# Optimization experiments

Hardware: AMD Instinct MI355X
Metric: run time of the kernel (lower is better)

## Reference

```python
import jax, jax.numpy as jnp
import numpy as np

NUM_HEADS = 12

def _rotate_half(t):
    t1, t2 = jnp.split(t, 2, axis=-1)
    return jnp.concatenate([-t2, t1], axis=-1)

def _rope_apply(t, sin, cos):
    # t: [B,H,N,Dh]; sin/cos: [N,Dh] broadcast over B,H
    return t * cos + _rotate_half(t) * sin


def setup_inputs() -> dict:
    key = jax.random.key(0)
    ks = jax.random.split(key, 6)
    B, N, D = 2, 2048, 768
    Dh = D // NUM_HEADS
    return {
        "x": jax.random.normal(ks[0], (B, N, D), dtype=jnp.float32),
        "sin": jax.random.uniform(ks[1], (N, Dh), dtype=jnp.float32),
        "cos": jax.random.uniform(ks[2], (N, Dh), dtype=jnp.float32),
        "qkv_w": jax.random.normal(ks[3], (3 * D, D), dtype=jnp.float32) * (D ** -0.5),
        "proj_w": jax.random.normal(ks[4], (D, D), dtype=jnp.float32) * (D ** -0.5),
        "proj_b": jax.random.normal(ks[5], (D,), dtype=jnp.float32),
    }


def reference(x, sin, cos, qkv_w, proj_w, proj_b):
    B, N, D = x.shape
    H = NUM_HEADS
    Dh = D // H
    scale = Dh ** -0.5
    # fused QKV projection (qkv_bias=False)
    qkv = jnp.einsum("bnd,ed->bne", x, qkv_w)              # [B,N,3D]
    qkv = qkv.reshape(B, N, 3, H, Dh)
    q = jnp.transpose(qkv[:, :, 0], (0, 2, 1, 3))          # [B,H,N,Dh]
    k = jnp.transpose(qkv[:, :, 1], (0, 2, 1, 3))
    v = jnp.transpose(qkv[:, :, 2], (0, 2, 1, 3))
    # inline RoPE (prefix = 0: sin/cos cover all N positions)
    q = _rope_apply(q, sin, cos)
    k = _rope_apply(k, sin, cos)
    # scaled dot-product attention
    scores = jnp.einsum("bhqd,bhkd->bhqk", q, k) * scale   # [B,H,N,N]
    attn = jax.nn.softmax(scores, axis=-1)
    out = jnp.einsum("bhqk,bhkd->bhqd", attn, v)           # [B,H,N,Dh]
    out = jnp.transpose(out, (0, 2, 1, 3)).reshape(B, N, D)
    # output projection
    return jnp.einsum("bnd,ed->bne", out, proj_w) + proj_b
```

## Files before the change

### kernel.cpp

```cpp
#include <hip/hip_runtime.h>
#include <hip/hip_bf16.h>
#include <stdint.h>


typedef unsigned short u16;
typedef __attribute__((ext_vector_type(8))) short s16x8;
typedef __attribute__((ext_vector_type(4))) short s16x4;
typedef __attribute__((ext_vector_type(4))) float f32x4;

#define MFMA16(a, b, c) __builtin_amdgcn_mfma_f32_16x16x32_bf16((a), (b), (c), 0, 0, 0)

__device__ __forceinline__ f32x4 mfma_k16(s16x4 a, s16x4 b, f32x4 c) {
    asm("s_nop 3\n\tv_mfma_f32_16x16x16_bf16 %0, %1, %2, %0"
        : "+v"(c) : "v"(a), "v"(b));
    return c;
}

__device__ __forceinline__ u16 f2bf(float f) {
    uint32_t u = __float_as_uint(f);
    u = u + 0x7fffu + ((u >> 16) & 1u);
    return (u16)(u >> 16);
}
__device__ __forceinline__ uint32_t pk2(float lo, float hi) {
    return (uint32_t)f2bf(lo) | ((uint32_t)f2bf(hi) << 16);
}
__device__ __forceinline__ uint32_t pk2t(float lo, float hi) {
    return __builtin_amdgcn_perm(__float_as_uint(hi), __float_as_uint(lo),
                                 0x07060302u);
}
__device__ __forceinline__ float fexp2(float x) { return __builtin_amdgcn_exp2f(x); }

__device__ __forceinline__ void gload16(const void* g, void* l) {
    __builtin_amdgcn_global_load_lds(
        (const __attribute__((address_space(1))) unsigned int*)g,
        (__attribute__((address_space(3))) unsigned int*)l,
        16, 0, 0);
}

__global__ __launch_bounds__(256)
void k_cvt3(const float* __restrict__ s0, const float* __restrict__ s1,
            const float* __restrict__ s2, u16* __restrict__ dst,
            int a, int ab, int tot)
{
    const int i = blockIdx.x * 256 + threadIdx.x;
    if (i >= tot) return;
    const float4* src;
    if (i < a)       src = (const float4*)s0 + i;
    else if (i < ab) src = (const float4*)s1 + (i - a);
    else             src = (const float4*)s2 + (i - ab);
    const float4 v = *src;
    ushort4 o;
    o.x = f2bf(v.x); o.y = f2bf(v.y); o.z = f2bf(v.z); o.w = f2bf(v.w);
    ((ushort4*)dst)[i] = o;
}

__global__ __launch_bounds__(256, 2)
void k_qkv_rope(const u16* __restrict__ X,
                const u16* __restrict__ W,
                const float* __restrict__ SIN,
                const float* __restrict__ COS,
                u16* __restrict__ qws, u16* __restrict__ kws, u16* __restrict__ vtws)
{
    __shared__ u16 smem[17408];
    u16* const As0 = smem;
    u16* const Bs0 = smem + 8192;

    const int t  = threadIdx.x;
    const int l  = t & 63;
    const int w  = t >> 6;
    const int cl = l & 15, gh = l >> 4;
    const int brow = blockIdx.x * 128;
    const int bcol = blockIdx.y * 128;
    const int wr = (w >> 1) * 64;
    const int wc = (w & 1) * 64;

    const int srow = w * 16 + (l >> 2);
    const int scol = (((l & 3) ^ ((l >> 3) & 3)) * 8);
    const u16* gA = X + (size_t)(brow + srow) * 768 + scol;
    const u16* gB = W + (size_t)(bcol + srow) * 768 + scol;

    const int csw = ((cl >> 1) & 3);

    f32x4 acc[4][4] = {};

    gload16(gA,            As0 + w * 512);
    gload16(gA + 64 * 768, As0 + 2048 + w * 512);
    gload16(gB,            Bs0 + w * 512);
    gload16(gB + 64 * 768, Bs0 + 2048 + w * 512);
    __syncthreads();

    for (int kt = 0; kt < 24; ++kt) {
        const int cur = kt & 1;
        if (kt + 1 < 24) {
            const int k0 = (kt + 1) * 32;
            u16* An = As0 + (cur ^ 1) * 4096;
            u16* Bn = Bs0 + (cur ^ 1) * 4096;
            gload16(gA + k0,            An + w * 512);
            gload16(gA + k0 + 64 * 768, An + 2048 + w * 512);
            gload16(gB + k0,            Bn + w * 512);
            gload16(gB + k0 + 64 * 768, Bn + 2048 + w * 512);
        }
        const char* Ac = (const char*)(As0 + cur * 4096);
        const char* Bc = (const char*)(Bs0 + cur * 4096);
        s16x8 af[4], bv[4];
        #pragma unroll
        for (int m = 0; m < 4; ++m) {
            const int row = wr + m * 16 + cl;
            af[m] = *(const s16x8*)(Ac + row * 64 + ((gh ^ csw) << 4));
        }
        #pragma unroll
        for (int n = 0; n < 4; ++n) {
            const int row = wc + n * 16 + cl;
            bv[n] = *(const s16x8*)(Bc + row * 64 + ((gh ^ csw) << 4));
        }
        #pragma unroll
        for (int m = 0; m < 4; ++m)
            #pragma unroll
            for (int n = 0; n < 4; ++n)
                acc[m][n] = MFMA16(af[m], bv[n], acc[m][n]);
        __syncthreads();
    }

    if (blockIdx.y >= 12) {
        u16* const Vt = smem;
        #pragma unroll
        for (int m = 0; m < 4; ++m)
            #pragma unroll
            for (int jj = 0; jj < 4; ++jj) {
                const int rowl = wr + m * 16 + gh * 4 + jj;
                #pragma unroll
                for (int n = 0; n < 4; ++n)
                    Vt[(wc + n * 16 + cl) * 136 + rowl] = f2bf(acc[m][n][jj]);
            }
        __syncthreads();
        const int dhcol = t >> 1;
        const int c     = t & 1;
        const int gcol  = bcol + dhcol;
        const int h     = (gcol >> 6) - 24;
        const int dh    = gcol & 63;
        const int b     = brow >> 11;
        const int tok0  = (brow & 2047) + c * 64;
        u16* dst = vtws + ((size_t)(b * 12 + h) * 64 + dh) * 2048 + tok0;
        const uint4* src = (const uint4*)((const char*)Vt + dhcol * 272 + c * 128);
        #pragma unroll
        for (int j = 0; j < 8; ++j)
            ((uint4*)dst)[j] = src[j];
    } else {
        const int seg   = (bcol + wc) >> 6;
        const int which = seg / 12;
        const int h     = seg % 12;
        const float qscl = (which == 0) ? 0.1803368801111244f : 1.0f;
        u16* outp = (which == 0) ? qws : kws;

        #pragma unroll
        for (int m = 0; m < 4; ++m) {
            #pragma unroll
            for (int jj = 0; jj < 4; ++jj) {
                const int row = brow + wr + m * 16 + gh * 4 + jj;
                const int b   = row >> 11;
                const int tok = row & 2047;
                u16* orow = outp + ((size_t)(b * 12 + h) * 2048 + tok) * 64;
                const float* srow2 = SIN + tok * 64;
                const float* crow2 = COS + tok * 64;
                #pragma unroll
                for (int n = 0; n < 4; ++n) {
                    const int dh = n * 16 + cl;
                    const float v = acc[m][n][jj];
                    const float partner = (n < 2) ? -acc[m][n + 2][jj] : acc[m][n - 2][jj];
                    orow[dh] = f2bf((v * crow2[dh] + partner * srow2[dh]) * qscl);
                }
            }
        }
    }
}

__global__ __launch_bounds__(256, 3)
void k_attn(const u16* __restrict__ Qg, const u16* __restrict__ Kg,
            const u16* __restrict__ VTg, u16* __restrict__ Og)
{
    __shared__ u16 Ks[2][64 * 64];
    __shared__ u16 Vs[2][64 * 64];

    const int t  = threadIdx.x;
    const int l  = t & 63;
    const int w  = t >> 6;
    const int cl = l & 15, gh = l >> 4;

    const int i  = blockIdx.x;
    const int bh = (i & 7) * 3 + ((i >> 3) % 3);
    const int qt = i / 24;
    const int qb = qt * 64;

    const u16* Q  = Qg  + (size_t)bh * 2048 * 64;
    const char* Kb  = (const char*)(Kg  + (size_t)bh * 2048 * 64);
    const char* VTb = (const char*)(VTg + (size_t)bh * 64 * 2048);

    s16x8 qf[4][2];
    #pragma unroll
    for (int m = 0; m < 4; ++m)
        #pragma unroll
        for (int ks = 0; ks < 2; ++ks)
            qf[m][ks] = *(const s16x8*)(Q + (((qb + m * 16 + cl) << 6) + ks * 32 + gh * 8));

    f32x4 o[4][4] = {};
    float lrun[4] = {};

    const int srow8 = l >> 3;
    const int scolb = (((l & 7) ^ srow8) << 4);
    const int rsw = (cl & 7) << 4;

    {
        #pragma unroll
        for (int c = 0; c < 2; ++c) {
            const int s = c * 4 + w;
            const int grow = s * 8 + srow8;
            gload16(Kb  + grow * 128 + scolb,  &Ks[0][s * 512]);
            gload16(VTb + grow * 4096 + scolb, &Vs[0][s * 512]);
        }
    }
    __syncthreads();

    for (int kt = 0; kt < 32; ++kt) {
        const int cur = kt & 1;

        if (kt + 1 < 32) {
            const int nb = (kt + 1) * 64;
            #pragma unroll
            for (int c = 0; c < 2; ++c) {
                const int s = c * 4 + w;
                const int grow = s * 8 + srow8;
                gload16(Kb  + (nb + grow) * 128 + scolb,    &Ks[cur ^ 1][s * 512]);
                gload16(VTb + grow * 4096 + nb * 2 + scolb, &Vs[cur ^ 1][s * 512]);
            }
        }

        const char* kl = (const char*)Ks[cur];
        const char* vl = (const char*)Vs[cur];
        s16x8 kf[2];
        s16x4 vf[4];
        #pragma unroll
        for (int ks = 0; ks < 2; ++ks)
            kf[ks] = *(const s16x8*)(kl + (w * 16 + cl) * 128 + ((ks * 64 + gh * 16) ^ rsw));
        #pragma unroll
        for (int n = 0; n < 4; ++n)
            vf[n] = *(const s16x4*)(vl + (n * 16 + cl) * 128 + ((w * 32 + gh * 8) ^ rsw));

        f32x4 st[4];
        #pragma unroll
        for (int m = 0; m < 4; ++m)
            #pragma unroll
            for (int jj = 0; jj < 4; ++jj)
                st[m][jj] = -12.f;
        #pragma unroll
        for (int m = 0; m < 4; ++m)
            #pragma unroll
            for (int ks = 0; ks < 2; ++ks)
                st[m] = MFMA16(kf[ks], qf[m][ks], st[m]);

        union { uint32_t u[2]; s16x4 v; } pd[4];
        #pragma unroll
        for (int m = 0; m < 4; ++m) {
            const float p0 = fexp2(st[m][0]);
            const float p1 = fexp2(st[m][1]);
            const float p2 = fexp2(st[m][2]);
            const float p3 = fexp2(st[m][3]);
            lrun[m] += (p0 + p1) + (p2 + p3);
            pd[m].u[0] = pk2t(p0, p1);
            pd[m].u[1] = pk2t(p2, p3);
        }

        #pragma unroll
        for (int n = 0; n < 4; ++n)
            #pragma unroll
            for (int m = 0; m < 4; ++m)
                o[n][m] = mfma_k16(vf[n], pd[m].v, o[n][m]);

        __syncthreads();
    }

    f32x4* OL = (f32x4*)&Ks[0][0];
    float*  ML = (float*)&Vs[0][0];
    const int b = bh / 12, h = bh % 12;

    #pragma unroll
    for (int m = 0; m < 4; ++m) {
        float lr = lrun[m];
        lr += __shfl_xor(lr, 16);
        lr += __shfl_xor(lr, 32);
        ML[(m * 4 + w) * 64 + l] = lr;
    }

    #pragma unroll
    for (int m = 0; m < 4; ++m) {
        __syncthreads();
        #pragma unroll
        for (int n = 0; n < 4; ++n)
            OL[(n * 4 + w) * 64 + l] = o[n][m];
        __syncthreads();
        f32x4 oacc = OL[(w * 4 + 0) * 64 + l];
        oacc += OL[(w * 4 + 1) * 64 + l];
        oacc += OL[(w * 4 + 2) * 64 + l];
        oacc += OL[(w * 4 + 3) * 64 + l];
        const float lt = ML[(m * 4 + 0) * 64 + l] + ML[(m * 4 + 1) * 64 + l]
                       + ML[(m * 4 + 2) * 64 + l] + ML[(m * 4 + 3) * 64 + l];
        const float inv = 1.0f / lt;
        const int tok = qb + m * 16 + cl;
        u16* orow = Og + ((size_t)(b * 2048 + tok)) * 768 + h * 64 + w * 16 + gh * 4;
        uint2 pkv;
        pkv.x = pk2(oacc[0] * inv, oacc[1] * inv);
        pkv.y = pk2(oacc[2] * inv, oacc[3] * inv);
        *(uint2*)orow = pkv;
    }
}

__global__ __launch_bounds__(256, 2)
void k_proj(const u16* __restrict__ A,
            const u16* __restrict__ W,
            const float* __restrict__ BIAS,
            float* __restrict__ OUT)
{
    __shared__ u16 smem[16384];
    u16* const As0 = smem;
    u16* const Bs0 = smem + 8192;

    const int t  = threadIdx.x;
    const int l  = t & 63;
    const int w  = t >> 6;
    const int cl = l & 15, gh = l >> 4;
    const int brow = blockIdx.x * 128;
    const int bcol = blockIdx.y * 128;
    const int wr = (w >> 1) * 64;
    const int wc = (w & 1) * 64;

    const int srow = w * 16 + (l >> 2);
    const int scol = (((l & 3) ^ ((l >> 3) & 3)) * 8);
    const u16* gA = A + (size_t)(brow + srow) * 768 + scol;
    const u16* gB = W + (size_t)(bcol + srow) * 768 + scol;
    const int csw = ((cl >> 1) & 3);

    f32x4 acc[4][4] = {};

    gload16(gA,            As0 + w * 512);
    gload16(gA + 64 * 768, As0 + 2048 + w * 512);
    gload16(gB,            Bs0 + w * 512);
    gload16(gB + 64 * 768, Bs0 + 2048 + w * 512);
    __syncthreads();

    for (int kt = 0; kt < 24; ++kt) {
        const int cur = kt & 1;
        if (kt + 1 < 24) {
            const int k0 = (kt + 1) * 32;
            u16* An = As0 + (cur ^ 1) * 4096;
            u16* Bn = Bs0 + (cur ^ 1) * 4096;
            gload16(gA + k0,            An + w * 512);
            gload16(gA + k0 + 64 * 768, An + 2048 + w * 512);
            gload16(gB + k0,            Bn + w * 512);
            gload16(gB + k0 + 64 * 768, Bn + 2048 + w * 512);
        }
        const char* Ac = (const char*)(As0 + cur * 4096);
        const char* Bc = (const char*)(Bs0 + cur * 4096);
        s16x8 af[4], bv[4];
        #pragma unroll
        for (int m = 0; m < 4; ++m) {
            const int row = wr + m * 16 + cl;
            af[m] = *(const s16x8*)(Ac + row * 64 + ((gh ^ csw) << 4));
        }
        #pragma unroll
        for (int n = 0; n < 4; ++n) {
            const int row = wc + n * 16 + cl;
            bv[n] = *(const s16x8*)(Bc + row * 64 + ((gh ^ csw) << 4));
        }
        #pragma unroll
        for (int m = 0; m < 4; ++m)
            #pragma unroll
            for (int n = 0; n < 4; ++n)
                acc[m][n] = MFMA16(af[m], bv[n], acc[m][n]);
        __syncthreads();
    }

    #pragma unroll
    for (int m = 0; m < 4; ++m) {
        #pragma unroll
        for (int jj = 0; jj < 4; ++jj) {
            const int row = brow + wr + m * 16 + gh * 4 + jj;
            #pragma unroll
            for (int n = 0; n < 4; ++n) {
                const int col = bcol + wc + n * 16 + cl;
                OUT[(size_t)row * 768 + col] = acc[m][n][jj] + BIAS[col];
            }
        }
    }
}

extern "C" void kernel_launch(void* const* d_in, const int* in_sizes, int n_in,
                              void* d_out, int out_size, void* d_ws, size_t ws_size,
                              hipStream_t stream)
{
    const float* x     = (const float*)d_in[0];
    const float* sinp  = (const float*)d_in[1];
    const float* cosp  = (const float*)d_in[2];
    const float* qkv_w = (const float*)d_in[3];
    const float* projw = (const float*)d_in[4];
    const float* projb = (const float*)d_in[5];
    float* out = (float*)d_out;

    const size_t N_X  = (size_t)4096 * 768;
    const size_t N_WQ = (size_t)2304 * 768;
    const size_t N_WP = (size_t)768 * 768;
    const size_t SEG  = (size_t)2 * 12 * 2048 * 64;

    u16* xbf   = (u16*)d_ws;
    u16* wqkv  = xbf + N_X;
    u16* wproj = wqkv + N_WQ;
    u16* qws   = wproj + N_WP;
    u16* kws   = qws + SEG;
    u16* vtws  = kws + SEG;
    u16* aws   = vtws + SEG;

    const int a   = (int)(N_X / 4);
    const int ab  = (int)((N_X + N_WQ) / 4);
    const int tot = (int)((N_X + N_WQ + N_WP) / 4);
    k_cvt3<<<(tot + 255) / 256, 256, 0, stream>>>(x, qkv_w, projw, xbf, a, ab, tot);

    k_qkv_rope<<<dim3(32, 18), 256, 0, stream>>>(xbf, wqkv, sinp, cosp, qws, kws, vtws);
    k_attn    <<<768, 256, 0, stream>>>(qws, kws, vtws, aws);
    k_proj    <<<dim3(32, 6),  256, 0, stream>>>(aws, wproj, projb, out);
}
```

Baseline: 93.97 us.

## Triple-buffer K/V tiles in attention with prefetch distance of two

The attention kernel's K/V shared-memory ring grows from two stages to three, and tiles are now prefetched two iterations ahead. The full __syncthreads is replaced with a partial vmcnt wait plus a raw barrier, so one tile's loads can stay in flight across the barrier. This is meant to hide global-load latency better. In exchange, LDS use rises from 32KB to 48KB per block, which may limit the 3-blocks-per-CU occupancy target.

```diff
diff --git a/kernel.cpp b/kernel.cpp
--- a/kernel.cpp
+++ b/kernel.cpp
@@ -178,8 +178,8 @@
 void k_attn(const u16* __restrict__ Qg, const u16* __restrict__ Kg,
             const u16* __restrict__ VTg, u16* __restrict__ Og)
 {
-    __shared__ u16 Ks[2][64 * 64];
-    __shared__ u16 Vs[2][64 * 64];
+    __shared__ u16 Ks[3][64 * 64];
+    __shared__ u16 Vs[3][64 * 64];
 
     const int t  = threadIdx.x;
     const int l  = t & 63;
@@ -209,33 +209,32 @@
     const int scolb = (((l & 7) ^ srow8) << 4);
     const int rsw = (cl & 7) << 4;
 
-    {
-        #pragma unroll
-        for (int c = 0; c < 2; ++c) {
-            const int s = c * 4 + w;
-            const int grow = s * 8 + srow8;
-            gload16(Kb  + grow * 128 + scolb,  &Ks[0][s * 512]);
-            gload16(VTb + grow * 4096 + scolb, &Vs[0][s * 512]);
-        }
-    }
-    __syncthreads();
-
+#define STAGE(T, KB, VB)                                                      \
+    {                                                                         \
+        const int nb_ = (T) * 64;                                             \
+        _Pragma("unroll")                                                     \
+        for (int c = 0; c < 2; ++c) {                                         \
+            const int s = c * 4 + w;                                          \
+            const int grow = s * 8 + srow8;                                   \
+            gload16(Kb  + (nb_ + grow) * 128 + scolb,    &(KB)[s * 512]);     \
+            gload16(VTb + grow * 4096 + nb_ * 2 + scolb, &(VB)[s * 512]);     \
+        }                                                                     \
+    }
+
+    STAGE(0, Ks[0], Vs[0])
+    STAGE(1, Ks[1], Vs[1])
+    asm volatile("s_waitcnt vmcnt(4)" ::: "memory");
+    __builtin_amdgcn_s_barrier();
+
+    int ci = 0;
     for (int kt = 0; kt < 32; ++kt) {
-        const int cur = kt & 1;
-
-        if (kt + 1 < 32) {
-            const int nb = (kt + 1) * 64;
-            #pragma unroll
-            for (int c = 0; c < 2; ++c) {
-                const int s = c * 4 + w;
-                const int grow = s * 8 + srow8;
-                gload16(Kb  + (nb + grow) * 128 + scolb,    &Ks[cur ^ 1][s * 512]);
-                gload16(VTb + grow * 4096 + nb * 2 + scolb, &Vs[cur ^ 1][s * 512]);
-            }
-        }
-
-        const char* kl = (const char*)Ks[cur];
-        const char* vl = (const char*)Vs[cur];
+        if (kt + 2 < 32) {
+            const int ii = (ci + 2 >= 3) ? ci - 1 : ci + 2;
+            STAGE(kt + 2, Ks[ii], Vs[ii])
+        }
+
+        const char* kl = (const char*)Ks[ci];
+        const char* vl = (const char*)Vs[ci];
         s16x8 kf[2];
         s16x4 vf[4];
         #pragma unroll
@@ -275,8 +274,13 @@
             for (int m = 0; m < 4; ++m)
                 o[n][m] = mfma_k16(vf[n], pd[m].v, o[n][m]);
 
-        __syncthreads();
-    }
+        if (kt < 30) asm volatile("s_waitcnt vmcnt(4)" ::: "memory");
+        else         asm volatile("s_waitcnt vmcnt(0)" ::: "memory");
+        __builtin_amdgcn_s_barrier();
+
+        ci = (ci == 2) ? 0 : ci + 1;
+    }
+#undef STAGE
 
     f32x4* OL = (f32x4*)&Ks[0][0];
     float*  ML = (float*)&Vs[0][0];
```

Measured after the change: 93.23 us. No clear change (-0.8%).
